# Kernel optimization log

Measured on AMD Instinct MI355X. Metric: run time of the kernel, lower is better.

The kernel has to match this reference:

```python
import jax, jax.numpy as jnp
import numpy as np

B, T = 2048, 32          # batch, max utterance length
V, H, A = 32000, 1024, 1000  # vocab, embedding_size, num_actions


def setup_inputs() -> dict:
    key = jax.random.key(0)
    ks = jax.random.split(key, 6)
    s = 0.02
    return {
        "utterance": jax.random.randint(ks[0], (B, T), 0, V, dtype=jnp.int32),
        "global_idxes": jnp.arange(B, dtype=jnp.int32),
        "emb_w": jax.random.normal(ks[1], (V, H), jnp.float32) * s,
        "w_ih": jax.random.normal(ks[2], (3 * H, H), jnp.float32) * s,
        "w_hh": jax.random.normal(ks[3], (3 * H, H), jnp.float32) * s,
        "b_ih": jnp.zeros((3 * H,), jnp.float32),
        "b_hh": jnp.zeros((3 * H,), jnp.float32),
        "h1_w": jax.random.normal(ks[4], (A, H), jnp.float32) * s,
        "h1_b": jnp.zeros((A,), jnp.float32),
    }


def _gru_cell(x, h, w_ih, w_hh, b_ih, b_hh):
    # PyTorch GRUCell: gate order r, z, n along the 3H axis
    gi = x @ w_ih.T + b_ih   # [B, 3H]
    gh = h @ w_hh.T + b_hh   # [B, 3H]
    ir, iz, inn = jnp.split(gi, 3, axis=-1)
    hr, hz, hn = jnp.split(gh, 3, axis=-1)
    r = jax.nn.sigmoid(ir + hr)
    z = jax.nn.sigmoid(iz + hz)
    n = jnp.tanh(inn + r * hn)
    return (1.0 - z) * n + z * h


def reference(utterance, global_idxes, emb_w, w_ih, w_hh, b_ih, b_hh, h1_w, h1_b):
    # Sieve semantics: a row stays alive until it emits token 0; the state is
    # updated at the step where the 0 token is consumed (inclusive), then frozen.
    batch = utterance.shape[0]
    hdim = emb_w.shape[1]

    def step(carry, tok_t):
        state, alive = carry
        emb = emb_w[tok_t]                              # [B, H] embedding lookup
        new_state = _gru_cell(emb, state, w_ih, w_hh, b_ih, b_hh)
        state = jnp.where(alive[:, None], new_state, state)
        alive = alive & (tok_t != 0)
        return (state, alive), None

    init = (jnp.zeros((batch, hdim), emb_w.dtype), jnp.ones((batch,), bool))
    (state, _), _ = jax.lax.scan(step, init, utterance.T)  # scan over time

    action_logits = state @ h1_w.T + h1_b                  # [B, A]
    action_probs = jax.nn.softmax(action_logits, axis=-1)
    return action_probs
```

## Files before the change

### kernel.cpp

```cpp
#include <hip/hip_runtime.h>
#include <cstdint>
#include <cstddef>

#define B_  2048
#define T_  32
#define V_  32000
#define H_  1024
#define A_  1000
#define H3  3072

typedef short short8 __attribute__((ext_vector_type(8)));
typedef float f32x4  __attribute__((ext_vector_type(4)));

typedef __attribute__((address_space(1))) void* as1v;
typedef __attribute__((address_space(3))) void* as3v;

__device__ __forceinline__ unsigned short f2bf(float f) {
  union { float f; unsigned u; } v; v.f = f;
  unsigned r = v.u + 0x7FFFu + ((v.u >> 16) & 1u);
  return (unsigned short)(r >> 16);
}
__device__ __forceinline__ float bf2f(unsigned short s) {
  union { unsigned u; float f; } v; v.u = ((unsigned)s) << 16;
  return v.f;
}
__device__ __forceinline__ float sigmoidf(float x) {
  return 1.f / (1.f + __expf(-x));
}


__global__ void conv_bf16(const float* __restrict__ src, unsigned short* __restrict__ dst, int n4) {
  int i = blockIdx.x * blockDim.x + threadIdx.x;
  if (i >= n4) return;
  float4 v = ((const float4*)src)[i];
  ushort4 o;
  o.x = f2bf(v.x); o.y = f2bf(v.y); o.z = f2bf(v.z); o.w = f2bf(v.w);
  ((ushort4*)dst)[i] = o;
}

__global__ void conv_h1w(const float* __restrict__ src, unsigned short* __restrict__ dst) {
  int i = blockIdx.x * blockDim.x + threadIdx.x;
  if (i >= 1024 * 1024) return;
  int row = i >> 10;
  dst[i] = (row < A_) ? f2bf(src[i]) : (unsigned short)0;
}

__global__ void init_state(float* __restrict__ state, unsigned short* __restrict__ hbf0) {
  int i = blockIdx.x * blockDim.x + threadIdx.x;
  if (i < B_ * H_) { state[i] = 0.f; hbf0[i] = 0; }
}

__global__ void prep(const int* __restrict__ utt, unsigned* __restrict__ alivemask,
                     int* __restrict__ uttT) {
  int b = blockIdx.x * blockDim.x + threadIdx.x;
  if (b >= B_) return;
  unsigned mask = 0, alive = 1;
  #pragma unroll
  for (int t = 0; t < T_; t++) {
    int tk = utt[b * T_ + t];
    mask |= alive << t;
    if (tk == 0) alive = 0;
    uttT[t * B_ + b] = tk;
  }
  alivemask[b] = mask;
}

__global__ void __launch_bounds__(256) gemm_ew(
    const unsigned short* __restrict__ Abase,
    const unsigned short* __restrict__ W,
    const float* __restrict__ bias,
    unsigned short* __restrict__ Cw)
{
  __shared__ __align__(16) unsigned short lA[128 * 64];
  __shared__ __align__(16) unsigned short lB[128 * 64];
  const int tid  = threadIdx.x;
  const int lane = tid & 63;
  const int wv   = tid >> 6;
  const int wr   = (wv >> 1) * 64;
  const int wc   = (wv & 1) * 64;
  const int lm   = lane & 15;
  const int lq   = lane >> 4;
  const int bx   = blockIdx.x, by = blockIdx.y;

  f32x4 acc[4][4];
  #pragma unroll
  for (int i = 0; i < 4; i++)
    #pragma unroll
    for (int j = 0; j < 4; j++)
      acc[i][j] = (f32x4){0.f, 0.f, 0.f, 0.f};

  for (int kt = 0; kt < H_; kt += 64) {
    __syncthreads();
    #pragma unroll
    for (int r = 0; r < 4; r++) {
      int li  = r * 256 + tid;
      int row = li >> 3;
      int gc  = (li & 7) ^ (row & 7);
      const unsigned short* ga = Abase + (size_t)(by * 128 + row) * H_ + kt + gc * 8;
      __builtin_amdgcn_global_load_lds((as1v)ga, (as3v)(&lA[(size_t)li * 8]), 16, 0, 0);
      const unsigned short* gb = W + (size_t)(bx * 128 + row) * H_ + kt + gc * 8;
      __builtin_amdgcn_global_load_lds((as1v)gb, (as3v)(&lB[(size_t)li * 8]), 16, 0, 0);
    }
    __syncthreads();
    #pragma unroll
    for (int kk = 0; kk < 2; kk++) {
      const int cs = (((kk << 2) | lq) ^ (lm & 7)) << 3;
      short8 af[4], bf[4];
      #pragma unroll
      for (int i = 0; i < 4; i++)
        af[i] = *(const short8*)&lA[(wr + i * 16 + lm) * 64 + cs];
      #pragma unroll
      for (int j = 0; j < 4; j++)
        bf[j] = *(const short8*)&lB[(wc + j * 16 + lm) * 64 + cs];
      #pragma unroll
      for (int i = 0; i < 4; i++)
        #pragma unroll
        for (int j = 0; j < 4; j++)
          acc[i][j] = __builtin_amdgcn_mfma_f32_16x16x32_bf16(af[i], bf[j], acc[i][j], 0, 0, 0);
    }
  }
  #pragma unroll
  for (int i = 0; i < 4; i++) {
    int row0 = by * 128 + wr + i * 16 + lq * 4;
    #pragma unroll
    for (int j = 0; j < 4; j++) {
      int col = bx * 128 + wc + j * 16 + lm;
      float bv = bias[col];
      #pragma unroll
      for (int rg = 0; rg < 4; rg++)
        Cw[(size_t)(row0 + rg) * H3 + col] = f2bf(acc[i][j][rg] + bv);
    }
  }
}

__global__ void __launch_bounds__(256) gemm_final(
    const unsigned short* __restrict__ Abase,
    const unsigned short* __restrict__ W,
    float* __restrict__ C)
{
  __shared__ __align__(16) unsigned short lA[128 * 64];
  __shared__ __align__(16) unsigned short lB[128 * 64];
  const int tid  = threadIdx.x;
  const int lane = tid & 63;
  const int wv   = tid >> 6;
  const int wr   = (wv >> 1) * 64;
  const int wc   = (wv & 1) * 64;
  const int lm   = lane & 15;
  const int lq   = lane >> 4;
  const int bx   = blockIdx.x, by = blockIdx.y;

  f32x4 acc[4][4];
  #pragma unroll
  for (int i = 0; i < 4; i++)
    #pragma unroll
    for (int j = 0; j < 4; j++)
      acc[i][j] = (f32x4){0.f, 0.f, 0.f, 0.f};

  for (int kt = 0; kt < H_; kt += 64) {
    __syncthreads();
    #pragma unroll
    for (int r = 0; r < 4; r++) {
      int li  = r * 256 + tid;
      int row = li >> 3;
      int gc  = (li & 7) ^ (row & 7);
      const unsigned short* ga = Abase + (size_t)(by * 128 + row) * H_ + kt + gc * 8;
      __builtin_amdgcn_global_load_lds((as1v)ga, (as3v)(&lA[(size_t)li * 8]), 16, 0, 0);
      const unsigned short* gb = W + (size_t)(bx * 128 + row) * H_ + kt + gc * 8;
      __builtin_amdgcn_global_load_lds((as1v)gb, (as3v)(&lB[(size_t)li * 8]), 16, 0, 0);
    }
    __syncthreads();
    #pragma unroll
    for (int kk = 0; kk < 2; kk++) {
      const int cs = (((kk << 2) | lq) ^ (lm & 7)) << 3;
      short8 af[4], bf[4];
      #pragma unroll
      for (int i = 0; i < 4; i++)
        af[i] = *(const short8*)&lA[(wr + i * 16 + lm) * 64 + cs];
      #pragma unroll
      for (int j = 0; j < 4; j++)
        bf[j] = *(const short8*)&lB[(wc + j * 16 + lm) * 64 + cs];
      #pragma unroll
      for (int i = 0; i < 4; i++)
        #pragma unroll
        for (int j = 0; j < 4; j++)
          acc[i][j] = __builtin_amdgcn_mfma_f32_16x16x32_bf16(af[i], bf[j], acc[i][j], 0, 0, 0);
    }
  }
  #pragma unroll
  for (int i = 0; i < 4; i++) {
    int row0 = by * 128 + wr + i * 16 + lq * 4;
    #pragma unroll
    for (int j = 0; j < 4; j++) {
      int col = bx * 128 + wc + j * 16 + lm;
      #pragma unroll
      for (int rg = 0; rg < 4; rg++)
        C[(size_t)(row0 + rg) * 1024 + col] = acc[i][j][rg];
    }
  }
}

__global__ void __launch_bounds__(256) step_fused(
    const unsigned short* __restrict__ EW,
    const int* __restrict__ uttT, int t,
    const unsigned short* __restrict__ hin,
    const unsigned short* __restrict__ whh_bf,
    const float* __restrict__ bhh,
    float* __restrict__ state,
    unsigned short* __restrict__ hout,
    const unsigned* __restrict__ amask)
{
  __shared__ __align__(16) unsigned short lA[64 * 64];
  __shared__ __align__(16) unsigned short lB[3 * 64 * 64];

  const int tid  = threadIdx.x;
  const int lane = tid & 63;
  const int wv   = tid >> 6;
  const int lm   = lane & 15;
  const int lq   = lane >> 4;
  const int hx   = blockIdx.x;
  const int bb   = blockIdx.y;

  int tokr[4];
  #pragma unroll
  for (int rg = 0; rg < 4; rg++)
    tokr[rg] = uttT[t * B_ + bb * 64 + wv * 16 + lq * 4 + rg];

  float hreg[4][4];
  float gir[4][4], giz[4][4], gin[4][4];
  #pragma unroll
  for (int j = 0; j < 4; j++) {
    int col = hx * 64 + j * 16 + lm;
    #pragma unroll
    for (int rg = 0; rg < 4; rg++) {
      int row = bb * 64 + wv * 16 + lq * 4 + rg;
      hreg[j][rg] = state[(size_t)row * H_ + col];
      const unsigned short* ep = EW + (size_t)tokr[rg] * H3 + col;
      gir[j][rg] = bf2f(ep[0]);
      giz[j][rg] = bf2f(ep[H_]);
      gin[j][rg] = bf2f(ep[2 * H_]);
    }
  }

  f32x4 acc[3][4];
  #pragma unroll
  for (int g = 0; g < 3; g++)
    #pragma unroll
    for (int j = 0; j < 4; j++)
      acc[g][j] = (f32x4){0.f, 0.f, 0.f, 0.f};

  for (int kt = 0; kt < H_; kt += 64) {
    __syncthreads();
    #pragma unroll
    for (int it = 0; it < 2; it++) {
      int li  = it * 256 + tid;
      int row = li >> 3;
      int gc  = (li & 7) ^ (row & 7);
      const unsigned short* ga = hin + (size_t)(bb * 64 + row) * H_ + kt + gc * 8;
      __builtin_amdgcn_global_load_lds((as1v)ga, (as3v)(&lA[(size_t)li * 8]), 16, 0, 0);
    }
    #pragma unroll
    for (int gg = 0; gg < 6; gg++) {
      int li  = gg * 256 + tid;
      int g   = li >> 9;
      int row = (li >> 3) & 63;
      int gc  = (li & 7) ^ (row & 7);
      const unsigned short* gb = whh_bf + (size_t)((g << 10) + hx * 64 + row) * H_ + kt + gc * 8;
      __builtin_amdgcn_global_load_lds((as1v)gb, (as3v)(&lB[(size_t)li * 8]), 16, 0, 0);
    }
    __syncthreads();
    #pragma unroll
    for (int kk = 0; kk < 2; kk++) {
      const int cs = (((kk << 2) | lq) ^ (lm & 7)) << 3;
      short8 af = *(const short8*)&lA[(wv * 16 + lm) * 64 + cs];
      #pragma unroll
      for (int g = 0; g < 3; g++) {
        #pragma unroll
        for (int j = 0; j < 4; j++) {
          short8 bf = *(const short8*)&lB[g * 4096 + (j * 16 + lm) * 64 + cs];
          acc[g][j] = __builtin_amdgcn_mfma_f32_16x16x32_bf16(af, bf, acc[g][j], 0, 0, 0);
        }
      }
    }
  }

  #pragma unroll
  for (int j = 0; j < 4; j++) {
    int col = hx * 64 + j * 16 + lm;
    float bhr = bhh[col];
    float bhz = bhh[H_ + col];
    float bhn = bhh[2 * H_ + col];
    #pragma unroll
    for (int rg = 0; rg < 4; rg++) {
      int row = bb * 64 + wv * 16 + lq * 4 + rg;
      float r = sigmoidf(gir[j][rg] + acc[0][j][rg] + bhr);
      float z = sigmoidf(giz[j][rg] + acc[1][j][rg] + bhz);
      float n = tanhf(gin[j][rg] + r * (acc[2][j][rg] + bhn));
      float h = hreg[j][rg];
      float nh = (1.f - z) * n + z * h;
      float o = ((amask[row] >> t) & 1u) ? nh : h;
      size_t si = (size_t)row * H_ + col;
      state[si] = o;
      hout[si] = f2bf(o);
    }
  }
}

__global__ void __launch_bounds__(256) softmax_k(const float* __restrict__ logits,
                                                 const float* __restrict__ h1b,
                                                 float* __restrict__ out)
{
  int b = blockIdx.x;
  int tid = threadIdx.x;
  __shared__ float red[8];
  float v[4];
  float lmax = -3.4e38f;
  #pragma unroll
  for (int k = 0; k < 4; k++) {
    int j = tid + k * 256;
    float x = (j < A_) ? (logits[(size_t)b * 1024 + j] + h1b[j]) : -3.4e38f;
    v[k] = x;
    lmax = fmaxf(lmax, x);
  }
  #pragma unroll
  for (int off = 1; off < 64; off <<= 1) lmax = fmaxf(lmax, __shfl_xor(lmax, off, 64));
  if ((tid & 63) == 0) red[tid >> 6] = lmax;
  __syncthreads();
  lmax = fmaxf(fmaxf(red[0], red[1]), fmaxf(red[2], red[3]));
  float s = 0.f;
  #pragma unroll
  for (int k = 0; k < 4; k++) {
    int j = tid + k * 256;
    float e = (j < A_) ? expf(v[k] - lmax) : 0.f;
    v[k] = e; s += e;
  }
  #pragma unroll
  for (int off = 1; off < 64; off <<= 1) s += __shfl_xor(s, off, 64);
  if ((tid & 63) == 0) red[4 + (tid >> 6)] = s;
  __syncthreads();
  s = red[4] + red[5] + red[6] + red[7];
  float inv = 1.f / s;
  #pragma unroll
  for (int k = 0; k < 4; k++) {
    int j = tid + k * 256;
    if (j < A_) out[(size_t)b * A_ + j] = v[k] * inv;
  }
}

extern "C" void kernel_launch(void* const* d_in, const int* in_sizes, int n_in,
                              void* d_out, int out_size, void* d_ws, size_t ws_size,
                              hipStream_t stream)
{
  (void)in_sizes; (void)n_in; (void)out_size; (void)ws_size;
  const int*   utt   = (const int*)d_in[0];
  const float* emb_w = (const float*)d_in[2];
  const float* w_ih  = (const float*)d_in[3];
  const float* w_hh  = (const float*)d_in[4];
  const float* b_ih  = (const float*)d_in[5];
  const float* b_hh  = (const float*)d_in[6];
  const float* h1_w  = (const float*)d_in[7];
  const float* h1_b  = (const float*)d_in[8];
  float* out = (float*)d_out;

  char* ws = (char*)d_ws;
  size_t off = 0;
  auto alloc = [&](size_t bytes) {
    void* p = ws + off;
    off += (bytes + 255) & ~(size_t)255;
    return p;
  };
  unsigned short* emb_bf = (unsigned short*)alloc((size_t)V_ * H_ * 2);
  unsigned short* wih_bf = (unsigned short*)alloc((size_t)H3 * H_ * 2);
  unsigned short* EW     = (unsigned short*)alloc((size_t)V_ * H3 * 2);
  unsigned short* whh_bf = (unsigned short*)alloc((size_t)H3 * H_ * 2);
  int*            uttT   = (int*)alloc((size_t)B_ * T_ * 4);
  unsigned*       amask  = (unsigned*)alloc((size_t)B_ * 4);

  char* ov = (char*)emb_bf;
  unsigned short* h1w_bf = (unsigned short*)(ov);
  float*          state  = (float*)(ov + 2097152);
  unsigned short* hbf0   = (unsigned short*)(ov + 10485760);
  unsigned short* hbf1   = (unsigned short*)(ov + 14680064);
  float*          logits = (float*)(ov + 18874368);

  int n4 = V_ * H_ / 4;
  conv_bf16<<<(n4 + 255) / 256, 256, 0, stream>>>(emb_w, emb_bf, n4);
  n4 = H3 * H_ / 4;
  conv_bf16<<<(n4 + 255) / 256, 256, 0, stream>>>(w_ih, wih_bf, n4);
  conv_bf16<<<(n4 + 255) / 256, 256, 0, stream>>>(w_hh, whh_bf, n4);
  prep<<<(B_ + 255) / 256, 256, 0, stream>>>(utt, amask, uttT);

  dim3 gew(H3 / 128, V_ / 128);
  gemm_ew<<<gew, 256, 0, stream>>>(emb_bf, wih_bf, b_ih, EW);

  conv_h1w<<<(1024 * 1024) / 256, 256, 0, stream>>>(h1_w, h1w_bf);
  init_state<<<(B_ * H_) / 256, 256, 0, stream>>>(state, hbf0);

  unsigned short* hb[2] = { hbf0, hbf1 };
  dim3 gst(16, 32);
  for (int t = 0; t < T_; t++) {
    step_fused<<<gst, 256, 0, stream>>>(EW, uttT, t, hb[t & 1], whh_bf, b_hh,
                                        state, hb[(t + 1) & 1], amask);
  }
  dim3 gf(1024 / 128, B_ / 128);
  gemm_final<<<gf, 256, 0, stream>>>(hb[0], h1w_bf, logits);
  softmax_k<<<B_, 256, 0, stream>>>(logits, h1_b, out);
}
```

Measured before the change: 1.453 ms.

## Double-buffer LDS tiles to overlap global loads with MFMA in GEMM kernels

Converts the LDS staging in gemm_ew, gemm_final and the per-timestep step_fused kernel to a two-buffer ping-pong scheme. The next K-tile is loaded with global_load_lds while MFMAs run on the current tile, leaving one barrier per iteration instead of two. The aim is to hide global memory latency behind matrix compute. The cost is double the LDS per block (64 KB), which lowers how many blocks fit on each CU.

```diff
diff --git a/kernel.cpp b/kernel.cpp
--- a/kernel.cpp
+++ b/kernel.cpp
@@ -71,8 +71,8 @@
     const float* __restrict__ bias,
     unsigned short* __restrict__ Cw)
 {
-  __shared__ __align__(16) unsigned short lA[128 * 64];
-  __shared__ __align__(16) unsigned short lB[128 * 64];
+  __shared__ __align__(16) unsigned short lA[2][128 * 64];
+  __shared__ __align__(16) unsigned short lB[2][128 * 64];
   const int tid  = threadIdx.x;
   const int lane = tid & 63;
   const int wv   = tid >> 6;
@@ -89,35 +89,41 @@
     for (int j = 0; j < 4; j++)
       acc[i][j] = (f32x4){0.f, 0.f, 0.f, 0.f};
 
-  for (int kt = 0; kt < H_; kt += 64) {
-    __syncthreads();
+  auto STAGE = [&](int buf, int kt) {
     #pragma unroll
     for (int r = 0; r < 4; r++) {
       int li  = r * 256 + tid;
       int row = li >> 3;
       int gc  = (li & 7) ^ (row & 7);
       const unsigned short* ga = Abase + (size_t)(by * 128 + row) * H_ + kt + gc * 8;
-      __builtin_amdgcn_global_load_lds((as1v)ga, (as3v)(&lA[(size_t)li * 8]), 16, 0, 0);
+      __builtin_amdgcn_global_load_lds((as1v)ga, (as3v)(&lA[buf][(size_t)li * 8]), 16, 0, 0);
       const unsigned short* gb = W + (size_t)(bx * 128 + row) * H_ + kt + gc * 8;
-      __builtin_amdgcn_global_load_lds((as1v)gb, (as3v)(&lB[(size_t)li * 8]), 16, 0, 0);
-    }
-    __syncthreads();
+      __builtin_amdgcn_global_load_lds((as1v)gb, (as3v)(&lB[buf][(size_t)li * 8]), 16, 0, 0);
+    }
+  };
+
+  STAGE(0, 0);
+  __syncthreads();
+  for (int kti = 0; kti < 16; kti++) {
+    const int cur = kti & 1;
+    if (kti < 15) STAGE(cur ^ 1, (kti + 1) * 64);
     #pragma unroll
     for (int kk = 0; kk < 2; kk++) {
       const int cs = (((kk << 2) | lq) ^ (lm & 7)) << 3;
       short8 af[4], bf[4];
       #pragma unroll
       for (int i = 0; i < 4; i++)
-        af[i] = *(const short8*)&lA[(wr + i * 16 + lm) * 64 + cs];
+        af[i] = *(const short8*)&lA[cur][(wr + i * 16 + lm) * 64 + cs];
       #pragma unroll
       for (int j = 0; j < 4; j++)
-        bf[j] = *(const short8*)&lB[(wc + j * 16 + lm) * 64 + cs];
+        bf[j] = *(const short8*)&lB[cur][(wc + j * 16 + lm) * 64 + cs];
       #pragma unroll
       for (int i = 0; i < 4; i++)
         #pragma unroll
         for (int j = 0; j < 4; j++)
           acc[i][j] = __builtin_amdgcn_mfma_f32_16x16x32_bf16(af[i], bf[j], acc[i][j], 0, 0, 0);
     }
+    __syncthreads();
   }
   #pragma unroll
   for (int i = 0; i < 4; i++) {
@@ -138,8 +144,8 @@
     const unsigned short* __restrict__ W,
     float* __restrict__ C)
 {
-  __shared__ __align__(16) unsigned short lA[128 * 64];
-  __shared__ __align__(16) unsigned short lB[128 * 64];
+  __shared__ __align__(16) unsigned short lA[2][128 * 64];
+  __shared__ __align__(16) unsigned short lB[2][128 * 64];
   const int tid  = threadIdx.x;
   const int lane = tid & 63;
   const int wv   = tid >> 6;
@@ -156,35 +162,41 @@
     for (int j = 0; j < 4; j++)
       acc[i][j] = (f32x4){0.f, 0.f, 0.f, 0.f};
 
-  for (int kt = 0; kt < H_; kt += 64) {
-    __syncthreads();
+  auto STAGE = [&](int buf, int kt) {
     #pragma unroll
     for (int r = 0; r < 4; r++) {
       int li  = r * 256 + tid;
       int row = li >> 3;
       int gc  = (li & 7) ^ (row & 7);
       const unsigned short* ga = Abase + (size_t)(by * 128 + row) * H_ + kt + gc * 8;
-      __builtin_amdgcn_global_load_lds((as1v)ga, (as3v)(&lA[(size_t)li * 8]), 16, 0, 0);
+      __builtin_amdgcn_global_load_lds((as1v)ga, (as3v)(&lA[buf][(size_t)li * 8]), 16, 0, 0);
       const unsigned short* gb = W + (size_t)(bx * 128 + row) * H_ + kt + gc * 8;
-      __builtin_amdgcn_global_load_lds((as1v)gb, (as3v)(&lB[(size_t)li * 8]), 16, 0, 0);
-    }
-    __syncthreads();
+      __builtin_amdgcn_global_load_lds((as1v)gb, (as3v)(&lB[buf][(size_t)li * 8]), 16, 0, 0);
+    }
+  };
+
+  STAGE(0, 0);
+  __syncthreads();
+  for (int kti = 0; kti < 16; kti++) {
+    const int cur = kti & 1;
+    if (kti < 15) STAGE(cur ^ 1, (kti + 1) * 64);
     #pragma unroll
     for (int kk = 0; kk < 2; kk++) {
       const int cs = (((kk << 2) | lq) ^ (lm & 7)) << 3;
       short8 af[4], bf[4];
       #pragma unroll
       for (int i = 0; i < 4; i++)
-        af[i] = *(const short8*)&lA[(wr + i * 16 + lm) * 64 + cs];
+        af[i] = *(const short8*)&lA[cur][(wr + i * 16 + lm) * 64 + cs];
       #pragma unroll
       for (int j = 0; j < 4; j++)
-        bf[j] = *(const short8*)&lB[(wc + j * 16 + lm) * 64 + cs];
+        bf[j] = *(const short8*)&lB[cur][(wc + j * 16 + lm) * 64 + cs];
       #pragma unroll
       for (int i = 0; i < 4; i++)
         #pragma unroll
         for (int j = 0; j < 4; j++)
           acc[i][j] = __builtin_amdgcn_mfma_f32_16x16x32_bf16(af[i], bf[j], acc[i][j], 0, 0, 0);
     }
+    __syncthreads();
   }
   #pragma unroll
   for (int i = 0; i < 4; i++) {
@@ -209,8 +221,8 @@
     unsigned short* __restrict__ hout,
     const unsigned* __restrict__ amask)
 {
-  __shared__ __align__(16) unsigned short lA[64 * 64];
-  __shared__ __align__(16) unsigned short lB[3 * 64 * 64];
+  __shared__ __align__(16) unsigned short lA[2][64 * 64];
+  __shared__ __align__(16) unsigned short lB[2][3 * 64 * 64];
 
   const int tid  = threadIdx.x;
   const int lane = tid & 63;
@@ -220,6 +232,28 @@
   const int hx   = blockIdx.x;
   const int bb   = blockIdx.y;
 
+  auto STAGE = [&](int buf, int kt) {
+    #pragma unroll
+    for (int it = 0; it < 2; it++) {
+      int li  = it * 256 + tid;
+      int row = li >> 3;
+      int gc  = (li & 7) ^ (row & 7);
+      const unsigned short* ga = hin + (size_t)(bb * 64 + row) * H_ + kt + gc * 8;
+      __builtin_amdgcn_global_load_lds((as1v)ga, (as3v)(&lA[buf][(size_t)li * 8]), 16, 0, 0);
+    }
+    #pragma unroll
+    for (int gg = 0; gg < 6; gg++) {
+      int li  = gg * 256 + tid;
+      int g   = li >> 9;
+      int row = (li >> 3) & 63;
+      int gc  = (li & 7) ^ (row & 7);
+      const unsigned short* gb = whh_bf + (size_t)((g << 10) + hx * 64 + row) * H_ + kt + gc * 8;
+      __builtin_amdgcn_global_load_lds((as1v)gb, (as3v)(&lB[buf][(size_t)li * 8]), 16, 0, 0);
+    }
+  };
+
+  STAGE(0, 0);
+
   int tokr[4];
   #pragma unroll
   for (int rg = 0; rg < 4; rg++)
@@ -248,39 +282,24 @@
     for (int j = 0; j < 4; j++)
       acc[g][j] = (f32x4){0.f, 0.f, 0.f, 0.f};
 
-  for (int kt = 0; kt < H_; kt += 64) {
-    __syncthreads();
-    #pragma unroll
-    for (int it = 0; it < 2; it++) {
-      int li  = it * 256 + tid;
-      int row = li >> 3;
-      int gc  = (li & 7) ^ (row & 7);
-      const unsigned short* ga = hin + (size_t)(bb * 64 + row) * H_ + kt + gc * 8;
-      __builtin_amdgcn_global_load_lds((as1v)ga, (as3v)(&lA[(size_t)li * 8]), 16, 0, 0);
-    }
-    #pragma unroll
-    for (int gg = 0; gg < 6; gg++) {
-      int li  = gg * 256 + tid;
-      int g   = li >> 9;
-      int row = (li >> 3) & 63;
-      int gc  = (li & 7) ^ (row & 7);
-      const unsigned short* gb = whh_bf + (size_t)((g << 10) + hx * 64 + row) * H_ + kt + gc * 8;
-      __builtin_amdgcn_global_load_lds((as1v)gb, (as3v)(&lB[(size_t)li * 8]), 16, 0, 0);
-    }
-    __syncthreads();
+  __syncthreads();
+  for (int kti = 0; kti < 16; kti++) {
+    const int cur = kti & 1;
+    if (kti < 15) STAGE(cur ^ 1, (kti + 1) * 64);
     #pragma unroll
     for (int kk = 0; kk < 2; kk++) {
       const int cs = (((kk << 2) | lq) ^ (lm & 7)) << 3;
-      short8 af = *(const short8*)&lA[(wv * 16 + lm) * 64 + cs];
+      short8 af = *(const short8*)&lA[cur][(wv * 16 + lm) * 64 + cs];
       #pragma unroll
       for (int g = 0; g < 3; g++) {
         #pragma unroll
         for (int j = 0; j < 4; j++) {
-          short8 bf = *(const short8*)&lB[g * 4096 + (j * 16 + lm) * 64 + cs];
+          short8 bf = *(const short8*)&lB[cur][g * 4096 + (j * 16 + lm) * 64 + cs];
           acc[g][j] = __builtin_amdgcn_mfma_f32_16x16x32_bf16(af, bf, acc[g][j], 0, 0, 0);
         }
       }
     }
+    __syncthreads();
   }
 
   #pragma unroll
```

Result: no change. 1.465 ms (+0.8%).

## Double-buffer LDS tiles in fused GRU step kernel to overlap loads with MFMA

Applied to the files above, without the earlier changes.

Makes the LDS A and B tiles in the per-step recurrent GEMM double-buffered. The next k-tile is prefetched with global_load_lds while MFMAs run on the current tile, and explicit vmcnt waits plus barriers replace the two syncthreads per iteration. The first stage is issued before the token, state and embedding gather so that this latency is also hidden. In exchange LDS use doubles to about 64KB per block, which may cut occupancy, and correctness now depends on the hand-written vmcnt count matching the 8 loads issued per stage.

```diff
diff --git a/kernel.cpp b/kernel.cpp
--- a/kernel.cpp
+++ b/kernel.cpp
@@ -209,8 +209,8 @@
     unsigned short* __restrict__ hout,
     const unsigned* __restrict__ amask)
 {
-  __shared__ __align__(16) unsigned short lA[64 * 64];
-  __shared__ __align__(16) unsigned short lB[3 * 64 * 64];
+  __shared__ __align__(16) unsigned short lA[2][64 * 64];
+  __shared__ __align__(16) unsigned short lB[2][3 * 64 * 64];
 
   const int tid  = threadIdx.x;
   const int lane = tid & 63;
@@ -220,6 +220,28 @@
   const int hx   = blockIdx.x;
   const int bb   = blockIdx.y;
 
+  auto STAGE = [&](int buf, int kt) {
+    #pragma unroll
+    for (int it = 0; it < 2; it++) {
+      int li  = it * 256 + tid;
+      int row = li >> 3;
+      int gc  = (li & 7) ^ (row & 7);
+      const unsigned short* ga = hin + (size_t)(bb * 64 + row) * H_ + kt + gc * 8;
+      __builtin_amdgcn_global_load_lds((as1v)ga, (as3v)(&lA[buf][(size_t)li * 8]), 16, 0, 0);
+    }
+    #pragma unroll
+    for (int gg = 0; gg < 6; gg++) {
+      int li  = gg * 256 + tid;
+      int g   = li >> 9;
+      int row = (li >> 3) & 63;
+      int gc  = (li & 7) ^ (row & 7);
+      const unsigned short* gb = whh_bf + (size_t)((g << 10) + hx * 64 + row) * H_ + kt + gc * 8;
+      __builtin_amdgcn_global_load_lds((as1v)gb, (as3v)(&lB[buf][(size_t)li * 8]), 16, 0, 0);
+    }
+  };
+
+  STAGE(0, 0);
+
   int tokr[4];
   #pragma unroll
   for (int rg = 0; rg < 4; rg++)
@@ -248,35 +270,29 @@
     for (int j = 0; j < 4; j++)
       acc[g][j] = (f32x4){0.f, 0.f, 0.f, 0.f};
 
-  for (int kt = 0; kt < H_; kt += 64) {
-    __syncthreads();
-    #pragma unroll
-    for (int it = 0; it < 2; it++) {
-      int li  = it * 256 + tid;
-      int row = li >> 3;
-      int gc  = (li & 7) ^ (row & 7);
-      const unsigned short* ga = hin + (size_t)(bb * 64 + row) * H_ + kt + gc * 8;
-      __builtin_amdgcn_global_load_lds((as1v)ga, (as3v)(&lA[(size_t)li * 8]), 16, 0, 0);
-    }
-    #pragma unroll
-    for (int gg = 0; gg < 6; gg++) {
-      int li  = gg * 256 + tid;
-      int g   = li >> 9;
-      int row = (li >> 3) & 63;
-      int gc  = (li & 7) ^ (row & 7);
-      const unsigned short* gb = whh_bf + (size_t)((g << 10) + hx * 64 + row) * H_ + kt + gc * 8;
-      __builtin_amdgcn_global_load_lds((as1v)gb, (as3v)(&lB[(size_t)li * 8]), 16, 0, 0);
-    }
-    __syncthreads();
+  #pragma unroll 1
+  for (int kti = 0; kti < 16; kti++) {
+    const int cur = kti & 1;
+    __builtin_amdgcn_s_barrier();
+    __builtin_amdgcn_sched_barrier(0);
+    if (kti < 15) {
+      STAGE(cur ^ 1, (kti + 1) * 64);
+      asm volatile("s_waitcnt vmcnt(8)" ::: "memory");
+    } else {
+      asm volatile("s_waitcnt vmcnt(0)" ::: "memory");
+    }
+    __builtin_amdgcn_sched_barrier(0);
+    __builtin_amdgcn_s_barrier();
+    __builtin_amdgcn_sched_barrier(0);
     #pragma unroll
     for (int kk = 0; kk < 2; kk++) {
       const int cs = (((kk << 2) | lq) ^ (lm & 7)) << 3;
-      short8 af = *(const short8*)&lA[(wv * 16 + lm) * 64 + cs];
+      short8 af = *(const short8*)&lA[cur][(wv * 16 + lm) * 64 + cs];
       #pragma unroll
       for (int g = 0; g < 3; g++) {
         #pragma unroll
         for (int j = 0; j < 4; j++) {
-          short8 bf = *(const short8*)&lB[g * 4096 + (j * 16 + lm) * 64 + cs];
+          short8 bf = *(const short8*)&lB[cur][g * 4096 + (j * 16 + lm) * 64 + cs];
           acc[g][j] = __builtin_amdgcn_mfma_f32_16x16x32_bf16(af, bf, acc[g][j], 0, 0, 0);
         }
       }
```

Result: faster. 1.372 ms (-5.6%).
